# Kernel optimization log

Hardware: AMD Instinct MI355X
Metric: run time of the kernel (lower is better)

Reference implementation:

```python
import jax, jax.numpy as jnp
import numpy as np

B, L, H, D = 16, 4096, 16, 64
HID = H * D


def setup_inputs() -> dict:
    key = jax.random.key(0)
    ks = jax.random.split(key, 10)
    w = lambda k: jax.random.normal(k, (HID, HID), jnp.float32) * 0.02
    return dict(
        hidden_states=jax.random.normal(ks[0], (B, 1, HID), jnp.float32),
        past_key=jax.random.normal(ks[1], (B, H, L, D), jnp.float32),
        past_value=jax.random.normal(ks[2], (B, H, L, D), jnp.float32),
        attention_mask=jnp.ones((B, L), jnp.float32),
        cache_position=jax.random.randint(ks[3], (B, 1), 0, L, jnp.int32),
        Wq=w(ks[4]), bq=jnp.zeros((HID,), jnp.float32),
        Wk=w(ks[5]), bk=jnp.zeros((HID,), jnp.float32),
        Wv=w(ks[6]), bv=jnp.zeros((HID,), jnp.float32),
        Wo=w(ks[7]), bo=jnp.zeros((HID,), jnp.float32),
    )


def reference(hidden_states, past_key, past_value, attention_mask, cache_position,
              Wq, bq, Wk, bk, Wv, bv, Wo, bo):
    # projections: [B,1,HID]; torch Linear => x @ W.T + b
    q = hidden_states @ Wq.T + bq
    k = hidden_states @ Wk.T + bk
    v = hidden_states @ Wv.T + bv
    # [B,H,1,D]
    q = q.reshape(B, 1, H, D).transpose(0, 2, 1, 3)
    k_new = k.reshape(B, H, D)
    v_new = v.reshape(B, H, D)
    pos = cache_position[:, 0]  # [B]
    bidx = jnp.arange(B)
    # write new token K/V into cache at cache_position (per-batch)
    k_cache = past_key.at[bidx, :, pos].set(k_new)
    v_cache = past_value.at[bidx, :, pos].set(v_new)
    scale = jnp.float32(1.0) / jnp.sqrt(jnp.float32(D))
    scores = jnp.einsum('bhqd,bhkd->bhqk', q, k_cache) * scale  # [B,H,1,L]
    neg = jnp.finfo(scores.dtype).min
    scores = jnp.where(attention_mask[:, None, None, :] > 0, scores, neg)
    p = jax.nn.softmax(scores, axis=-1)
    ctx = jnp.einsum('bhqk,bhkd->bhqd', p, v_cache)  # [B,H,1,D]
    attn_output = ctx.transpose(0, 2, 1, 3).reshape(B, 1, HID) @ Wo.T + bo
    return attn_output, k_cache, v_cache
```

## Files before the change

kernel.cpp:

```cpp
#include <hip/hip_runtime.h>
#include <hip/hip_bf16.h>

#define BATCH 16
#define SEQL  4096
#define NH    16
#define HD    64
#define HID   1024
#define NCHUNK 8
#define CHUNK  (SEQL / NCHUNK)
#define KV_ELEMS (BATCH * NH * SEQL * HD)
#define PSTRIDE 68
#define C2 0.1803368801f

typedef float f4 __attribute__((ext_vector_type(4)));

__global__ __launch_bounds__(256) void proj_partial(
    const float* __restrict__ x,
    const float* __restrict__ W0,
    const float* __restrict__ W1,
    const float* __restrict__ W2,
    float* __restrict__ part)
{
    __shared__ float xs[BATCH * HID];
    const int t = threadIdx.x;
    for (int i = t; i < BATCH * HID; i += 256) xs[i] = x[i];
    __syncthreads();

    const float* W = (blockIdx.y == 0) ? W0 : ((blockIdx.y == 1) ? W1 : W2);
    const int otile = blockIdx.x;
    const int z     = blockIdx.z;
    const int og = t & 15;
    const int sl = t >> 4;
    const int obase = otile * 64 + og * 4;
    const int kbase = z * 256 + sl * 16;

    float acc[4][BATCH];
    #pragma unroll
    for (int oi = 0; oi < 4; ++oi)
        #pragma unroll
        for (int b = 0; b < BATCH; ++b) acc[oi][b] = 0.f;

    #pragma unroll
    for (int kk = 0; kk < 16; kk += 4) {
        const int k = kbase + kk;
        f4 w4[4];
        #pragma unroll
        for (int oi = 0; oi < 4; ++oi)
            w4[oi] = *(const f4*)&W[(size_t)(obase + oi) * HID + k];
        #pragma unroll
        for (int b = 0; b < BATCH; ++b) {
            f4 h4 = *(const f4*)&xs[b * HID + k];
            #pragma unroll
            for (int oi = 0; oi < 4; ++oi)
                acc[oi][b] += w4[oi].x * h4.x + w4[oi].y * h4.y
                            + w4[oi].z * h4.z + w4[oi].w * h4.w;
        }
    }

    __syncthreads();
    float* red = xs;
    #pragma unroll
    for (int oi = 0; oi < 4; ++oi)
        #pragma unroll
        for (int b = 0; b < BATCH; ++b)
            red[((sl * 16 + og) * 4 + oi) * 16 + b] = acc[oi][b];
    __syncthreads();

    #pragma unroll
    for (int u = 0; u < 4; ++u) {
        const int idx = t * 4 + u;
        const int o_local = idx >> 4;
        const int b = idx & 15;
        const int ogg = o_local >> 2, oii = o_local & 3;
        float s = 0.f;
        #pragma unroll
        for (int s2 = 0; s2 < 16; ++s2)
            s += red[((s2 * 16 + ogg) * 4 + oii) * 16 + b];
        part[(size_t)(blockIdx.y * 4 + z) * (BATCH * HID)
             + b * HID + otile * 64 + o_local] = s;
    }
}

__global__ __launch_bounds__(256) void reduce_qkv(
    const float* __restrict__ part,
    const float* __restrict__ bq, const float* __restrict__ bk,
    const float* __restrict__ bv, float* __restrict__ qkv)
{
    const int i = blockIdx.x * 256 + threadIdx.x;
    const int w = i >> 14;
    const int rem = i & 16383;
    const int o = rem & (HID - 1);
    float s = 0.f;
    #pragma unroll
    for (int z = 0; z < 4; ++z)
        s += part[(size_t)(w * 4 + z) * (BATCH * HID) + rem];
    const float* bias = (w == 0) ? bq : ((w == 1) ? bk : bv);
    qkv[i] = s + bias[o];
}

__global__ __launch_bounds__(256, 8) void attn_fused(
    const float* __restrict__ qkv,
    const float* __restrict__ past_k,
    const float* __restrict__ past_v,
    const float* __restrict__ mask,
    float* __restrict__ kout,
    float* __restrict__ vout,
    float* __restrict__ part)
{
    const int bh = blockIdx.x;
    const int c  = blockIdx.y;
    const int b  = bh >> 4;
    const int h  = bh & 15;
    const int t  = threadIdx.x;
    const int g  = t >> 4;
    const int j  = t & 15;

    const f4 q4 = *(const f4*)&qkv[b * HID + h * HD + j * 4];

    const size_t base = (size_t)bh * SEQL * HD;
    const float* __restrict__ pkb = past_k + base;
    const float* __restrict__ pvb = past_v + base;
    float* __restrict__ kob = kout + base;
    float* __restrict__ vob = vout + base;
    const float* __restrict__ mrow = mask + b * SEQL;

    float l = 0.f;
    f4 a4 = {0.f, 0.f, 0.f, 0.f};

    int r = c * CHUNK + g;
    #pragma unroll 1
    for (int it = 0; it < CHUNK / 64; ++it) {
        f4 k4[4], v4[4];
        float am[4];
        int ro[4];
        #pragma unroll
        for (int u = 0; u < 4; ++u) {
            const int rr = r + u * 16;
            ro[u] = rr * HD + (j << 2);
            k4[u] = __builtin_nontemporal_load((const f4*)(pkb + ro[u]));
            v4[u] = __builtin_nontemporal_load((const f4*)(pvb + ro[u]));
            am[u] = mrow[rr];
        }
        #pragma unroll
        for (int u = 0; u < 4; ++u) {
            __builtin_nontemporal_store(k4[u], (f4*)(kob + ro[u]));
            __builtin_nontemporal_store(v4[u], (f4*)(vob + ro[u]));
        }
        #pragma unroll
        for (int u = 0; u < 4; ++u) {
            float d = k4[u].x * q4.x + k4[u].y * q4.y
                    + k4[u].z * q4.z + k4[u].w * q4.w;
            d += __shfl_xor(d, 1);
            d += __shfl_xor(d, 2);
            d += __shfl_xor(d, 4);
            d += __shfl_xor(d, 8);
            float p = exp2f(d * C2);
            p = (am[u] > 0.f) ? p : 0.f;
            l += p;
            a4.x += p * v4[u].x;
            a4.y += p * v4[u].y;
            a4.z += p * v4[u].z;
            a4.w += p * v4[u].w;
        }
        r += 64;
    }

    __shared__ float sl_[16];
    __shared__ float sa[16][64];
    if (j == 0) sl_[g] = l;
    *(f4*)&sa[g][j * 4] = a4;
    __syncthreads();

    float* pr = part + ((size_t)bh * NCHUNK + c) * PSTRIDE;
    if (t < 64) {
        float A = 0.f;
        #pragma unroll
        for (int gg = 0; gg < 16; ++gg) A += sa[gg][t];
        pr[1 + t] = A;
    } else if (t == 64) {
        float L = 0.f;
        #pragma unroll
        for (int gg = 0; gg < 16; ++gg) L += sl_[gg];
        pr[0] = L;
    }
}

__global__ __launch_bounds__(64) void merge_fix(
    const float* __restrict__ qkv,
    const float* __restrict__ past_k,
    const float* __restrict__ past_v,
    const float* __restrict__ mask,
    const int*   __restrict__ cpos,
    float* __restrict__ kout,
    float* __restrict__ vout,
    const float* __restrict__ part,
    float* __restrict__ ctx)
{
    const int bh = blockIdx.x;
    const int b = bh >> 4, h = bh & 15;
    const int t = threadIdx.x;
    const int pos = cpos[b];

    const size_t rowoff = (size_t)bh * SEQL * HD + (size_t)pos * HD + t;
    const int qo = b * HID + h * HD + t;
    const float qd  = qkv[qo];
    const float knd = qkv[BATCH * HID + qo];
    const float vnd = qkv[2 * BATCH * HID + qo];
    const float ksd = past_k[rowoff];
    const float vsd = past_v[rowoff];

    kout[rowoff] = knd;
    vout[rowoff] = vnd;

    float dst = qd * ksd, dnw = qd * knd;
    #pragma unroll
    for (int sh = 1; sh < 64; sh <<= 1) {
        dst += __shfl_xor(dst, sh);
        dnw += __shfl_xor(dnw, sh);
    }
    const float am = mask[b * SEQL + pos];
    float ps = 0.f, pn = 0.f;
    if (am > 0.f) { ps = exp2f(dst * C2); pn = exp2f(dnw * C2); }

    const int cc0 = pos / CHUNK;
    float L = 0.f, A = 0.f;
    #pragma unroll
    for (int cc = 0; cc < NCHUNK; ++cc) {
        const float* pr = part + ((size_t)bh * NCHUNK + cc) * PSTRIDE;
        float Lc = pr[0];
        float Ac = pr[1 + t];
        if (cc == cc0) { Lc += pn - ps; Ac += pn * vnd - ps * vsd; }
        L += Lc;
        A += Ac;
    }
    ctx[bh * HD + t] = A / L;
}

__global__ __launch_bounds__(256) void reduce_out(
    const float* __restrict__ part, const float* __restrict__ bo,
    float* __restrict__ out)
{
    const int i = blockIdx.x * 256 + threadIdx.x;
    const int o = i & (HID - 1);
    float s = 0.f;
    #pragma unroll
    for (int z = 0; z < 4; ++z)
        s += part[(size_t)z * (BATCH * HID) + i];
    out[i] = s + bo[o];
}

extern "C" void kernel_launch(void* const* d_in, const int* in_sizes, int n_in,
                              void* d_out, int out_size, void* d_ws, size_t ws_size,
                              hipStream_t stream) {
    const float* hs   = (const float*)d_in[0];
    const float* pk   = (const float*)d_in[1];
    const float* pv   = (const float*)d_in[2];
    const float* mask = (const float*)d_in[3];
    const int*   cpos = (const int*)d_in[4];
    const float* Wq   = (const float*)d_in[5];
    const float* bq   = (const float*)d_in[6];
    const float* Wk   = (const float*)d_in[7];
    const float* bk   = (const float*)d_in[8];
    const float* Wv   = (const float*)d_in[9];
    const float* bv   = (const float*)d_in[10];
    const float* Wo   = (const float*)d_in[11];
    const float* bo   = (const float*)d_in[12];

    float* out_attn = (float*)d_out;
    float* kout = out_attn + BATCH * HID;
    float* vout = kout + KV_ELEMS;

    float* ws    = (float*)d_ws;
    float* qkv   = ws;
    float* ctx   = ws + 49152;
    float* apart = ws + 65536;
    float* ppart = ws + 204800;

    proj_partial<<<dim3(16, 3, 4), 256, 0, stream>>>(hs, Wq, Wk, Wv, ppart);
    reduce_qkv<<<dim3(192), 256, 0, stream>>>(ppart, bq, bk, bv, qkv);

    attn_fused<<<dim3(256, NCHUNK), 256, 0, stream>>>(qkv, pk, pv, mask,
                                                      kout, vout, apart);
    merge_fix<<<dim3(256), 64, 0, stream>>>(qkv, pk, pv, mask, cpos,
                                            kout, vout, apart, ctx);

    proj_partial<<<dim3(16, 1, 4), 256, 0, stream>>>(ctx, Wo, Wo, Wo, ppart);
    reduce_out<<<dim3(64), 256, 0, stream>>>(ppart, bo, out_attn);
}
```

Baseline: 229.6 us.

## Replace split-K projection plus reduce kernels with single wave-reduced GEMV kernel

```diff
diff --git a/kernel.cpp b/kernel.cpp
--- a/kernel.cpp
+++ b/kernel.cpp
@@ -14,88 +14,60 @@
 
 typedef float f4 __attribute__((ext_vector_type(4)));
 
-__global__ __launch_bounds__(256) void proj_partial(
+__global__ __launch_bounds__(256) void gemv3(
     const float* __restrict__ x,
-    const float* __restrict__ W0,
-    const float* __restrict__ W1,
+    const float* __restrict__ W0, const float* __restrict__ W1,
     const float* __restrict__ W2,
-    float* __restrict__ part)
+    const float* __restrict__ b0, const float* __restrict__ b1,
+    const float* __restrict__ b2,
+    float* __restrict__ out)
 {
     __shared__ float xs[BATCH * HID];
     const int t = threadIdx.x;
-    for (int i = t; i < BATCH * HID; i += 256) xs[i] = x[i];
+    {
+        const f4* src = (const f4*)x;
+        f4* dst = (f4*)xs;
+        #pragma unroll
+        for (int i = 0; i < (BATCH * HID / 4) / 256; ++i)
+            dst[t + i * 256] = src[t + i * 256];
+    }
     __syncthreads();
 
-    const float* W = (blockIdx.y == 0) ? W0 : ((blockIdx.y == 1) ? W1 : W2);
-    const int otile = blockIdx.x;
-    const int z     = blockIdx.z;
-    const int og = t & 15;
-    const int sl = t >> 4;
-    const int obase = otile * 64 + og * 4;
-    const int kbase = z * 256 + sl * 16;
-
-    float acc[4][BATCH];
-    #pragma unroll
-    for (int oi = 0; oi < 4; ++oi)
-        #pragma unroll
-        for (int b = 0; b < BATCH; ++b) acc[oi][b] = 0.f;
-
-    #pragma unroll
-    for (int kk = 0; kk < 16; kk += 4) {
-        const int k = kbase + kk;
-        f4 w4[4];
-        #pragma unroll
-        for (int oi = 0; oi < 4; ++oi)
-            w4[oi] = *(const f4*)&W[(size_t)(obase + oi) * HID + k];
+    const int which = blockIdx.x >> 8;
+    const int ob    = (blockIdx.x & 255) << 2;
+    const float* W    = (which == 0) ? W0 : ((which == 1) ? W1 : W2);
+    const float* bias = (which == 0) ? b0 : ((which == 1) ? b1 : b2);
+    const int col = t >> 6, lane = t & 63;
+    const int o = ob + col;
+    const float* wrow = W + (size_t)o * HID;
+
+    float acc[BATCH];
+    #pragma unroll
+    for (int b = 0; b < BATCH; ++b) acc[b] = 0.f;
+
+    #pragma unroll
+    for (int i = 0; i < 4; ++i) {
+        const int k = (lane << 2) + (i << 8);
+        const f4 w4 = *(const f4*)&wrow[k];
         #pragma unroll
         for (int b = 0; b < BATCH; ++b) {
-            f4 h4 = *(const f4*)&xs[b * HID + k];
-            #pragma unroll
-            for (int oi = 0; oi < 4; ++oi)
-                acc[oi][b] += w4[oi].x * h4.x + w4[oi].y * h4.y
-                            + w4[oi].z * h4.z + w4[oi].w * h4.w;
+            const f4 h4 = *(const f4*)&xs[b * HID + k];
+            acc[b] += w4.x * h4.x + w4.y * h4.y + w4.z * h4.z + w4.w * h4.w;
         }
     }
 
-    __syncthreads();
-    float* red = xs;
-    #pragma unroll
-    for (int oi = 0; oi < 4; ++oi)
+    #pragma unroll
+    for (int b = 0; b < BATCH; ++b) {
+        #pragma unroll
+        for (int sh = 1; sh < 64; sh <<= 1)
+            acc[b] += __shfl_xor(acc[b], sh);
+    }
+    if (lane == 0) {
+        const float bb = bias[o];
         #pragma unroll
         for (int b = 0; b < BATCH; ++b)
-            red[((sl * 16 + og) * 4 + oi) * 16 + b] = acc[oi][b];
-    __syncthreads();
-
-    #pragma unroll
-    for (int u = 0; u < 4; ++u) {
-        const int idx = t * 4 + u;
-        const int o_local = idx >> 4;
-        const int b = idx & 15;
-        const int ogg = o_local >> 2, oii = o_local & 3;
-        float s = 0.f;
-        #pragma unroll
-        for (int s2 = 0; s2 < 16; ++s2)
-            s += red[((s2 * 16 + ogg) * 4 + oii) * 16 + b];
-        part[(size_t)(blockIdx.y * 4 + z) * (BATCH * HID)
-             + b * HID + otile * 64 + o_local] = s;
-    }
-}
-
-__global__ __launch_bounds__(256) void reduce_qkv(
-    const float* __restrict__ part,
-    const float* __restrict__ bq, const float* __restrict__ bk,
-    const float* __restrict__ bv, float* __restrict__ qkv)
-{
-    const int i = blockIdx.x * 256 + threadIdx.x;
-    const int w = i >> 14;
-    const int rem = i & 16383;
-    const int o = rem & (HID - 1);
-    float s = 0.f;
-    #pragma unroll
-    for (int z = 0; z < 4; ++z)
-        s += part[(size_t)(w * 4 + z) * (BATCH * HID) + rem];
-    const float* bias = (w == 0) ? bq : ((w == 1) ? bk : bv);
-    qkv[i] = s + bias[o];
+            out[which * (BATCH * HID) + b * HID + o] = acc[b] + bb;
+    }
 }
 
 __global__ __launch_bounds__(256, 8) void attn_fused(
@@ -115,9 +87,9 @@
     const int g  = t >> 4;
     const int j  = t & 15;
 
-    const f4 q4 = *(const f4*)&qkv[b * HID + h * HD + j * 4];
-
-    const size_t base = (size_t)bh * SEQL * HD;
+    const f4 q4 = *(const f4*)&qkv[b * HID + h * HD + (j << 2)];
+
+    const size_t base = (size_t)bh * (SEQL * HD);
     const float* __restrict__ pkb = past_k + base;
     const float* __restrict__ pvb = past_v + base;
     float* __restrict__ kob = kout + base;
@@ -127,48 +99,53 @@
     float l = 0.f;
     f4 a4 = {0.f, 0.f, 0.f, 0.f};
 
-    int r = c * CHUNK + g;
+    int r0  = c * CHUNK + g;
+    int off = r0 * HD + (j << 2);
+
     #pragma unroll 1
-    for (int it = 0; it < CHUNK / 64; ++it) {
-        f4 k4[4], v4[4];
-        float am[4];
-        int ro[4];
-        #pragma unroll
-        for (int u = 0; u < 4; ++u) {
-            const int rr = r + u * 16;
-            ro[u] = rr * HD + (j << 2);
-            k4[u] = __builtin_nontemporal_load((const f4*)(pkb + ro[u]));
-            v4[u] = __builtin_nontemporal_load((const f4*)(pvb + ro[u]));
-            am[u] = mrow[rr];
-        }
-        #pragma unroll
-        for (int u = 0; u < 4; ++u) {
-            __builtin_nontemporal_store(k4[u], (f4*)(kob + ro[u]));
-            __builtin_nontemporal_store(v4[u], (f4*)(vob + ro[u]));
-        }
-        #pragma unroll
-        for (int u = 0; u < 4; ++u) {
-            float d = k4[u].x * q4.x + k4[u].y * q4.y
-                    + k4[u].z * q4.z + k4[u].w * q4.w;
-            d += __shfl_xor(d, 1);
-            d += __shfl_xor(d, 2);
-            d += __shfl_xor(d, 4);
-            d += __shfl_xor(d, 8);
-            float p = exp2f(d * C2);
-            p = (am[u] > 0.f) ? p : 0.f;
-            l += p;
-            a4.x += p * v4[u].x;
-            a4.y += p * v4[u].y;
-            a4.z += p * v4[u].z;
-            a4.w += p * v4[u].w;
-        }
-        r += 64;
+    for (int it = 0; it < CHUNK / 32; ++it) {
+        const int o1 = off + 16 * HD;
+        const f4 k0 = __builtin_nontemporal_load((const f4*)(pkb + off));
+        const f4 v0 = __builtin_nontemporal_load((const f4*)(pvb + off));
+        const f4 k1 = __builtin_nontemporal_load((const f4*)(pkb + o1));
+        const f4 v1 = __builtin_nontemporal_load((const f4*)(pvb + o1));
+        const float am0 = mrow[r0];
+        const float am1 = mrow[r0 + 16];
+        __builtin_nontemporal_store(k0, (f4*)(kob + off));
+        __builtin_nontemporal_store(v0, (f4*)(vob + off));
+        __builtin_nontemporal_store(k1, (f4*)(kob + o1));
+        __builtin_nontemporal_store(v1, (f4*)(vob + o1));
+
+        float d0 = k0.x * q4.x + k0.y * q4.y + k0.z * q4.z + k0.w * q4.w;
+        d0 += __shfl_xor(d0, 1);
+        d0 += __shfl_xor(d0, 2);
+        d0 += __shfl_xor(d0, 4);
+        d0 += __shfl_xor(d0, 8);
+        float p0 = exp2f(d0 * C2);
+        p0 = (am0 > 0.f) ? p0 : 0.f;
+        l += p0;
+        a4.x += p0 * v0.x; a4.y += p0 * v0.y;
+        a4.z += p0 * v0.z; a4.w += p0 * v0.w;
+
+        float d1 = k1.x * q4.x + k1.y * q4.y + k1.z * q4.z + k1.w * q4.w;
+        d1 += __shfl_xor(d1, 1);
+        d1 += __shfl_xor(d1, 2);
+        d1 += __shfl_xor(d1, 4);
+        d1 += __shfl_xor(d1, 8);
+        float p1 = exp2f(d1 * C2);
+        p1 = (am1 > 0.f) ? p1 : 0.f;
+        l += p1;
+        a4.x += p1 * v1.x; a4.y += p1 * v1.y;
+        a4.z += p1 * v1.z; a4.w += p1 * v1.w;
+
+        off += 32 * HD;
+        r0  += 32;
     }
 
     __shared__ float sl_[16];
     __shared__ float sa[16][64];
     if (j == 0) sl_[g] = l;
-    *(f4*)&sa[g][j * 4] = a4;
+    *(f4*)&sa[g][(j << 2)] = a4;
     __syncthreads();
 
     float* pr = part + ((size_t)bh * NCHUNK + c) * PSTRIDE;
@@ -201,7 +178,7 @@
     const int t = threadIdx.x;
     const int pos = cpos[b];
 
-    const size_t rowoff = (size_t)bh * SEQL * HD + (size_t)pos * HD + t;
+    const size_t rowoff = (size_t)bh * (SEQL * HD) + (size_t)pos * HD + t;
     const int qo = b * HID + h * HD + t;
     const float qd  = qkv[qo];
     const float knd = qkv[BATCH * HID + qo];
@@ -234,19 +211,6 @@
         A += Ac;
     }
     ctx[bh * HD + t] = A / L;
-}
-
-__global__ __launch_bounds__(256) void reduce_out(
-    const float* __restrict__ part, const float* __restrict__ bo,
-    float* __restrict__ out)
-{
-    const int i = blockIdx.x * 256 + threadIdx.x;
-    const int o = i & (HID - 1);
-    float s = 0.f;
-    #pragma unroll
-    for (int z = 0; z < 4; ++z)
-        s += part[(size_t)z * (BATCH * HID) + i];
-    out[i] = s + bo[o];
 }
 
 extern "C" void kernel_launch(void* const* d_in, const int* in_sizes, int n_in,
@@ -274,16 +238,13 @@
     float* qkv   = ws;
     float* ctx   = ws + 49152;
     float* apart = ws + 65536;
-    float* ppart = ws + 204800;
-
-    proj_partial<<<dim3(16, 3, 4), 256, 0, stream>>>(hs, Wq, Wk, Wv, ppart);
-    reduce_qkv<<<dim3(192), 256, 0, stream>>>(ppart, bq, bk, bv, qkv);
+
+    gemv3<<<dim3(768), 256, 0, stream>>>(hs, Wq, Wk, Wv, bq, bk, bv, qkv);
 
     attn_fused<<<dim3(256, NCHUNK), 256, 0, stream>>>(qkv, pk, pv, mask,
                                                       kout, vout, apart);
     merge_fix<<<dim3(256), 64, 0, stream>>>(qkv, pk, pv, mask, cpos,
                                             kout, vout, apart, ctx);
 
-    proj_partial<<<dim3(16, 1, 4), 256, 0, stream>>>(ctx, Wo, Wo, Wo, ppart);
-    reduce_out<<<dim3(64), 256, 0, stream>>>(ppart, bo, out_attn);
-}
+    gemv3<<<dim3(256), 256, 0, stream>>>(ctx, Wo, Wo, Wo, bo, bo, bo, out_attn);
+}
```

Result: faster. 222.8 us (-3.0%).
